# Optimization experiments

Hardware: AMD Instinct MI355X
Metric: run time of the kernel (lower is better)

The kernel has to match this reference:

```python
import jax, jax.numpy as jnp
import numpy as np

N_NODES = 50000
N_EDGES = 800000
N_GRAPHS = 64
IN_DIM = 108
HID = 128
OUT_DIM = 64


def setup_inputs() -> dict:
    key = jax.random.key(0)
    ks = jax.random.split(key, 10)
    x = jax.random.normal(ks[0], (N_NODES, IN_DIM - 1), dtype=jnp.float32)
    votes = jax.random.normal(ks[1], (N_NODES, 1), dtype=jnp.float32)
    edge_index = jax.random.randint(ks[2], (2, N_EDGES), 0, N_NODES, dtype=jnp.int64)
    batch = jnp.sort(jax.random.randint(ks[3], (N_NODES,), 0, N_GRAPHS, dtype=jnp.int64))
    # SAGEConv params (PyG defaults: mean aggr; lin_l has bias, lin_r has no bias)
    s1 = 1.0 / np.sqrt(IN_DIM)
    s2 = 1.0 / np.sqrt(HID)
    W1l = jax.random.uniform(ks[4], (IN_DIM, HID), jnp.float32, -s1, s1)
    b1 = jnp.zeros((HID,), jnp.float32)
    W1r = jax.random.uniform(ks[5], (IN_DIM, HID), jnp.float32, -s1, s1)
    W2l = jax.random.uniform(ks[6], (HID, OUT_DIM), jnp.float32, -s2, s2)
    b2 = jnp.zeros((OUT_DIM,), jnp.float32)
    W2r = jax.random.uniform(ks[7], (HID, OUT_DIM), jnp.float32, -s2, s2)
    return {"x": x, "votes": votes, "edge_index": edge_index, "batch": batch,
            "W1l": W1l, "b1": b1, "W1r": W1r, "W2l": W2l, "b2": b2, "W2r": W2r}


def _sage_conv(h, src, dst, Wl, b, Wr):
    # mean-aggregate neighbor features x_j at target i, then lin_l(agg) + lin_r(x_i)
    agg = jax.ops.segment_sum(h[src], dst, num_segments=h.shape[0])  # [N, d]
    deg = jax.ops.segment_sum(jnp.ones((src.shape[0],), h.dtype), dst,
                              num_segments=h.shape[0])
    agg = agg / jnp.maximum(deg, 1.0)[:, None]
    return agg @ Wl + b + h @ Wr


def reference(x, votes, edge_index, batch, W1l, b1, W1r, W2l, b2, W2r):
    src, dst = edge_index[0], edge_index[1]
    h = jnp.concatenate([x, votes], axis=1)              # [N, 108]
    h = jax.nn.relu(_sage_conv(h, src, dst, W1l, b1, W1r))  # [N, 128]
    h = _sage_conv(h, src, dst, W2l, b2, W2r)               # [N, 64]
    return jax.ops.segment_max(h, batch, num_segments=N_GRAPHS)  # [G, 64]
```

## Files before the change

### kernel.cpp

```cpp
#include <hip/hip_runtime.h>
#include <hip/hip_bf16.h>

#define IN_F 108
#define XD   107
#define HID  128
#define OUTD 64
#define SEG_NODES 64
#define BSH 6
#define BNODES 64
#define MAXBK 1024
#define EPB 4096
#define SRCMASK 0x03FFFFFF
#define BP1_N (8 * 7 * 64 * 8)
#define BP2_N (8 * 4 * 64 * 8)

typedef unsigned short ushort_t;
typedef unsigned int uint_t;
typedef __attribute__((ext_vector_type(8))) short bf16x8;
typedef __attribute__((ext_vector_type(4))) float f32x4;

__device__ inline void atomicMaxF(float* addr, float val) {
    if (val >= 0.f) atomicMax((int*)addr, __float_as_int(val));
    else            atomicMin((unsigned int*)addr, __float_as_uint(val));
}

__device__ inline ushort_t f2bf(float f) {
    uint_t b = __float_as_uint(f);
    return (ushort_t)((b + 0x7fffu + ((b >> 16) & 1u)) >> 16);
}

__global__ void init0_kernel(int* bcnt, int nbk, float* out, int n) {
    int i = blockIdx.x * 256 + threadIdx.x;
    if (i < nbk) bcnt[i] = 0;
    if (i < n) out[i] = -__builtin_inff();
}

__global__ __launch_bounds__(256) void bhist_kernel(const int* __restrict__ dst,
                                                    int* __restrict__ bcnt, int E, int nbk) {
    __shared__ int lh[MAXBK];
    for (int i = threadIdx.x; i < nbk; i += 256) lh[i] = 0;
    __syncthreads();
    int base = blockIdx.x * EPB;
    int end = min(base + EPB, E);
    for (int k = base + threadIdx.x; k < end; k += 256)
        atomicAdd(&lh[dst[k] >> BSH], 1);
    __syncthreads();
    for (int i = threadIdx.x; i < nbk; i += 256)
        if (lh[i] > 0) atomicAdd(&bcnt[i], lh[i]);
}

__global__ __launch_bounds__(64) void bscan_kernel(const int* __restrict__ bcnt,
                                                   int* __restrict__ bbase,
                                                   int* __restrict__ brsv,
                                                   int* __restrict__ row_start,
                                                   int nbk, int N, int E) {
    int lane = threadIdx.x;
    int carry = 0;
    for (int b = 0; b < nbk; b += 64) {
        int i = b + lane;
        int orig = (i < nbk) ? bcnt[i] : 0;
        int v = orig;
#pragma unroll
        for (int d = 1; d < 64; d <<= 1) {
            int t = __shfl_up(v, d);
            if (lane >= d) v += t;
        }
        if (i < nbk) {
            int ex = carry + v - orig;
            bbase[i] = ex;
            brsv[i] = ex;
        }
        carry += __shfl(v, 63);
    }
    if (lane == 0) {
        bbase[nbk] = E;
        row_start[N] = E;
    }
}

__global__ __launch_bounds__(256) void bscatter_kernel(const int* __restrict__ src,
                                                       const int* __restrict__ dst,
                                                       int* __restrict__ brsv,
                                                       uint_t* __restrict__ ebuf,
                                                       int E, int nbk) {
    __shared__ int lh[MAXBK];
    __shared__ int lofs[MAXBK];
    for (int i = threadIdx.x; i < nbk; i += 256) lh[i] = 0;
    __syncthreads();
    int base = blockIdx.x * EPB;
    int end = min(base + EPB, E);
    for (int k = base + threadIdx.x; k < end; k += 256)
        atomicAdd(&lh[dst[k] >> BSH], 1);
    __syncthreads();
    for (int i = threadIdx.x; i < nbk; i += 256)
        if (lh[i] > 0) lofs[i] = atomicAdd(&brsv[i], lh[i]);
    __syncthreads();
    for (int k = base + threadIdx.x; k < end; k += 256) {
        int d = dst[k];
        int pos = atomicAdd(&lofs[d >> BSH], 1);
        ebuf[pos] = (uint_t)src[k] | ((uint_t)(d & (BNODES - 1)) << 26);
    }
}

__global__ __launch_bounds__(256) void bbuild_kernel(const uint_t* __restrict__ ebuf,
                                                     const int* __restrict__ bbase,
                                                     int* __restrict__ row_start,
                                                     int* __restrict__ sorted_src,
                                                     int N) {
    __shared__ int nh[BNODES];
    __shared__ int cur[BNODES];
    int b = blockIdx.x;
    int e0 = bbase[b], e1 = bbase[b + 1];
    int nlo = b << BSH;
    int nloc = min(BNODES, N - nlo);
    if (threadIdx.x < BNODES) nh[threadIdx.x] = 0;
    __syncthreads();
    for (int k = e0 + threadIdx.x; k < e1; k += 256)
        atomicAdd(&nh[ebuf[k] >> 26], 1);
    __syncthreads();
    if (threadIdx.x < 64) {
        int lane = threadIdx.x;
        int orig = nh[lane];
        int v = orig;
#pragma unroll
        for (int d = 1; d < 64; d <<= 1) {
            int t = __shfl_up(v, d);
            if (lane >= d) v += t;
        }
        int ex = e0 + v - orig;
        cur[lane] = ex;
        if (lane < nloc) row_start[nlo + lane] = ex;
    }
    __syncthreads();
    for (int k = e0 + threadIdx.x; k < e1; k += 256) {
        uint_t e = ebuf[k];
        int pos = atomicAdd(&cur[e >> 26], 1);
        sorted_src[pos] = (int)(e & SRCMASK);
    }
}

__global__ void prep_kernel(const float* __restrict__ x, const float* __restrict__ votes,
                            const float* __restrict__ W1l, const float* __restrict__ W1r,
                            const float* __restrict__ W2l, const float* __restrict__ W2r,
                            ushort_t* __restrict__ xb, ushort_t* __restrict__ bp1,
                            ushort_t* __restrict__ bp2, int N) {
    int idx = blockIdx.x * 256 + threadIdx.x;
    if (idx < N * IN_F) {
        int n = idx / IN_F, f = idx - n * IN_F;
        float v = (f < XD) ? x[n * XD + f] : votes[n];
        xb[idx] = f2bf(v);
    }
    if (idx < BP1_N) {
        int j = idx & 7;
        int lane = (idx >> 3) & 63;
        int rest = idx >> 9;
        int ks = rest % 7;
        int ct = rest / 7;
        int k = ks * 32 + (lane >> 4) * 8 + j;
        int col = ct * 16 + (lane & 15);
        float v = 0.f;
        if (k < IN_F) v = W1l[k * HID + col];
        else if (k < 2 * IN_F) v = W1r[(k - IN_F) * HID + col];
        bp1[idx] = f2bf(v);
    }
    int i2 = idx - BP1_N;
    if (i2 >= 0 && i2 < BP2_N) {
        int j = i2 & 7;
        int lane = (i2 >> 3) & 63;
        int ks = (i2 >> 9) & 3;
        int ct = i2 >> 11;
        int k = ks * 32 + (lane >> 4) * 8 + j;
        int col = ct * 16 + (lane & 15);
        float v = (col < OUTD) ? W2l[k * OUTD + col] : W2r[k * OUTD + (col - OUTD)];
        bp2[i2] = f2bf(v);
    }
}

#define T1_M 32
#define A_STRIDE_US 232
#define A_STRIDE_U  116
#define H1_STRIDE_US 136
__global__ __launch_bounds__(256) void fused1_kernel(
        const ushort_t* __restrict__ xb,
        const int* __restrict__ row_start, const int* __restrict__ sorted_src,
        const ushort_t* __restrict__ bp1, const ushort_t* __restrict__ bp2,
        const float* __restrict__ b1,
        ushort_t* __restrict__ ub, float* __restrict__ vv, int N) {
    __shared__ uint_t smem[T1_M * A_STRIDE_U];
    int n0 = blockIdx.x * T1_M;
    const uint_t* xbu = (const uint_t*)xb;

    for (int i = threadIdx.x; i < T1_M * 54; i += 256) {
        int m = i / 54, c = i - m * 54;
        int n = n0 + m;
        smem[m * A_STRIDE_U + 54 + c] = (n < N) ? xbu[n * 54 + c] : 0u;
    }
    for (int i = threadIdx.x; i < T1_M * 4; i += 256) {
        int m = i >> 2, c = i & 3;
        smem[m * A_STRIDE_U + 108 + c] = 0u;
    }

    int lane = threadIdx.x & 63;
    int wid  = threadIdx.x >> 6;
    int h  = lane >> 5;
    int l2 = lane & 31;

    for (int it = 0; it < 8; ++it) {
        int m = wid * 8 + it;
        int node = n0 + m;
        float a0 = 0.f, a1 = 0.f, a2 = 0.f, a3 = 0.f;
        int deg = 0;
        if (node < N) {
            int rs = row_start[node], re = row_start[node + 1];
            deg = re - rs;
            for (int k0 = rs; k0 < re; k0 += 64) {
                int cnt = min(64, re - k0);
                int sl = sorted_src[k0 + min(lane, cnt - 1)];
                int t = 0;
                for (; t + 8 <= cnt; t += 8) {
                    int s0 = __shfl(sl, t + h);
                    int s1 = __shfl(sl, t + 2 + h);
                    int s2 = __shfl(sl, t + 4 + h);
                    int s3 = __shfl(sl, t + 6 + h);
                    if (l2 < 27) {
                        uint2 w0 = *(const uint2*)(xb + s0 * IN_F + 4 * l2);
                        uint2 w1 = *(const uint2*)(xb + s1 * IN_F + 4 * l2);
                        uint2 w2 = *(const uint2*)(xb + s2 * IN_F + 4 * l2);
                        uint2 w3 = *(const uint2*)(xb + s3 * IN_F + 4 * l2);
                        a0 += __uint_as_float(w0.x << 16) + __uint_as_float(w1.x << 16)
                            + __uint_as_float(w2.x << 16) + __uint_as_float(w3.x << 16);
                        a1 += __uint_as_float(w0.x & 0xffff0000u) + __uint_as_float(w1.x & 0xffff0000u)
                            + __uint_as_float(w2.x & 0xffff0000u) + __uint_as_float(w3.x & 0xffff0000u);
                        a2 += __uint_as_float(w0.y << 16) + __uint_as_float(w1.y << 16)
                            + __uint_as_float(w2.y << 16) + __uint_as_float(w3.y << 16);
                        a3 += __uint_as_float(w0.y & 0xffff0000u) + __uint_as_float(w1.y & 0xffff0000u)
                            + __uint_as_float(w2.y & 0xffff0000u) + __uint_as_float(w3.y & 0xffff0000u);
                    }
                }
                for (; t < cnt; t += 2) {
                    int tt = min(t + h, cnt - 1);
                    int s = __shfl(sl, tt);
                    if (t + h < cnt && l2 < 27) {
                        uint2 w = *(const uint2*)(xb + s * IN_F + 4 * l2);
                        a0 += __uint_as_float(w.x << 16);
                        a1 += __uint_as_float(w.x & 0xffff0000u);
                        a2 += __uint_as_float(w.y << 16);
                        a3 += __uint_as_float(w.y & 0xffff0000u);
                    }
                }
            }
        }
        a0 += __shfl_xor(a0, 32);
        a1 += __shfl_xor(a1, 32);
        a2 += __shfl_xor(a2, 32);
        a3 += __shfl_xor(a3, 32);
        if (node < N && l2 < 27) {
            float inv = 1.f / fmaxf((float)deg, 1.f);
            ushort4 p;
            p.x = f2bf(a0 * inv);
            p.y = f2bf(a1 * inv);
            p.z = f2bf(a2 * inv);
            p.w = f2bf(a3 * inv);
            *(ushort4*)((ushort_t*)smem + m * A_STRIDE_US + 4 * l2) = p;
        }
    }
    __syncthreads();

    int wrow = (wid & 1) << 4;
    int wcol = (wid >> 1) << 6;
    int arow = wrow + (lane & 15);
    int akoff = (lane >> 4) * 8;
    const ushort_t* sA = (const ushort_t*)smem;
    const bf16x8* bp1v = (const bf16x8*)bp1;

    f32x4 acc0 = {}, acc1 = {}, acc2_ = {}, acc3 = {};
    int ct0 = wcol >> 4;
#pragma unroll
    for (int ks = 0; ks < 7; ++ks) {
        bf16x8 af = *(const bf16x8*)(sA + arow * A_STRIDE_US + ks * 32 + akoff);
        bf16x8 bf0 = bp1v[((ct0 + 0) * 7 + ks) * 64 + lane];
        bf16x8 bf1 = bp1v[((ct0 + 1) * 7 + ks) * 64 + lane];
        bf16x8 bf2 = bp1v[((ct0 + 2) * 7 + ks) * 64 + lane];
        bf16x8 bf3 = bp1v[((ct0 + 3) * 7 + ks) * 64 + lane];
        acc0 = __builtin_amdgcn_mfma_f32_16x16x32_bf16(af, bf0, acc0, 0, 0, 0);
        acc1 = __builtin_amdgcn_mfma_f32_16x16x32_bf16(af, bf1, acc1, 0, 0, 0);
        acc2_ = __builtin_amdgcn_mfma_f32_16x16x32_bf16(af, bf2, acc2_, 0, 0, 0);
        acc3 = __builtin_amdgcn_mfma_f32_16x16x32_bf16(af, bf3, acc3, 0, 0, 0);
    }

    __syncthreads();
    ushort_t* sh1 = (ushort_t*)smem;
    {
        int colb = wcol + (lane & 15);
        int rowb = wrow + ((lane >> 4) << 2);
#pragma unroll
        for (int t = 0; t < 4; ++t) {
            f32x4 a = (t == 0) ? acc0 : (t == 1) ? acc1 : (t == 2) ? acc2_ : acc3;
            int col = colb + t * 16;
            float bj = b1[col];
#pragma unroll
            for (int r = 0; r < 4; ++r)
                sh1[(rowb + r) * H1_STRIDE_US + col] = f2bf(fmaxf(a[r] + bj, 0.f));
        }
    }
    __syncthreads();

    const bf16x8* bp2v = (const bf16x8*)bp2;
    f32x4 dcc0 = {}, dcc1 = {}, dcc2 = {}, dcc3 = {};
#pragma unroll
    for (int ks = 0; ks < 4; ++ks) {
        bf16x8 af = *(const bf16x8*)(sh1 + arow * H1_STRIDE_US + ks * 32 + akoff);
        bf16x8 bf0 = bp2v[((ct0 + 0) * 4 + ks) * 64 + lane];
        bf16x8 bf1 = bp2v[((ct0 + 1) * 4 + ks) * 64 + lane];
        bf16x8 bf2 = bp2v[((ct0 + 2) * 4 + ks) * 64 + lane];
        bf16x8 bf3 = bp2v[((ct0 + 3) * 4 + ks) * 64 + lane];
        dcc0 = __builtin_amdgcn_mfma_f32_16x16x32_bf16(af, bf0, dcc0, 0, 0, 0);
        dcc1 = __builtin_amdgcn_mfma_f32_16x16x32_bf16(af, bf1, dcc1, 0, 0, 0);
        dcc2 = __builtin_amdgcn_mfma_f32_16x16x32_bf16(af, bf2, dcc2, 0, 0, 0);
        dcc3 = __builtin_amdgcn_mfma_f32_16x16x32_bf16(af, bf3, dcc3, 0, 0, 0);
    }

    {
        int colb = wcol + (lane & 15);
        int rowb = wrow + ((lane >> 4) << 2);
#pragma unroll
        for (int t = 0; t < 4; ++t) {
            f32x4 a = (t == 0) ? dcc0 : (t == 1) ? dcc1 : (t == 2) ? dcc2 : dcc3;
            int col = colb + t * 16;
#pragma unroll
            for (int r = 0; r < 4; ++r) {
                int n = n0 + rowb + r;
                if (n < N) {
                    if (col < OUTD) ub[(n << 6) + col] = f2bf(a[r]);
                    else            vv[(n << 6) + (col - OUTD)] = a[r];
                }
            }
        }
    }
}

__global__ __launch_bounds__(256) void gatheru_kernel(
        const ushort_t* __restrict__ ub,
        const int* __restrict__ row_start, const int* __restrict__ sorted_src,
        float* __restrict__ aggu, int N) {
    int node = (blockIdx.x * 256 + threadIdx.x) >> 6;
    int lane = threadIdx.x & 63;
    if (node >= N) return;
    int rs = row_start[node], re = row_start[node + 1];
    int g  = lane >> 4;
    int l4 = lane & 15;
    float a0 = 0.f, a1 = 0.f, a2 = 0.f, a3 = 0.f;
    for (int k0 = rs; k0 < re; k0 += 64) {
        int cnt = min(64, re - k0);
        int sl = sorted_src[k0 + min(lane, cnt - 1)];
        int t = 0;
        for (; t + 8 <= cnt; t += 8) {
            int s0 = __shfl(sl, t + g);
            int s1 = __shfl(sl, t + 4 + g);
            uint2 w0 = *(const uint2*)(ub + (s0 << 6) + 4 * l4);
            uint2 w1 = *(const uint2*)(ub + (s1 << 6) + 4 * l4);
            a0 += __uint_as_float(w0.x << 16) + __uint_as_float(w1.x << 16);
            a1 += __uint_as_float(w0.x & 0xffff0000u) + __uint_as_float(w1.x & 0xffff0000u);
            a2 += __uint_as_float(w0.y << 16) + __uint_as_float(w1.y << 16);
            a3 += __uint_as_float(w0.y & 0xffff0000u) + __uint_as_float(w1.y & 0xffff0000u);
        }
        for (; t < cnt; t += 4) {
            int tt = min(t + g, cnt - 1);
            int s = __shfl(sl, tt);
            if (t + g < cnt) {
                uint2 w = *(const uint2*)(ub + (s << 6) + 4 * l4);
                a0 += __uint_as_float(w.x << 16);
                a1 += __uint_as_float(w.x & 0xffff0000u);
                a2 += __uint_as_float(w.y << 16);
                a3 += __uint_as_float(w.y & 0xffff0000u);
            }
        }
    }
    a0 += __shfl_xor(a0, 16); a0 += __shfl_xor(a0, 32);
    a1 += __shfl_xor(a1, 16); a1 += __shfl_xor(a1, 32);
    a2 += __shfl_xor(a2, 16); a2 += __shfl_xor(a2, 32);
    a3 += __shfl_xor(a3, 16); a3 += __shfl_xor(a3, 32);
    float inv = 1.f / fmaxf((float)(re - rs), 1.f);
    if (lane < 16) {
        *(float4*)(aggu + (node << 6) + 4 * lane) =
            make_float4(a0 * inv, a1 * inv, a2 * inv, a3 * inv);
    }
}

__global__ __launch_bounds__(256) void finalize_kernel(
        const float* __restrict__ aggu, const float* __restrict__ vv,
        const float* __restrict__ b2, const int* __restrict__ batch,
        float* __restrict__ out, int N) {
    int j  = threadIdx.x & 63;
    int nq = threadIdx.x >> 6;
    int n0 = blockIdx.x * SEG_NODES;
    float bj = b2[j];
    int curg = -1;
    float curm = -__builtin_inff();
    for (int m = nq; m < SEG_NODES; m += 4) {
        int n = n0 + m;
        if (n >= N) break;
        int g = batch[n];
        float v = aggu[(n << 6) + j] + vv[(n << 6) + j] + bj;
        if (g != curg) {
            if (curg >= 0) atomicMaxF(&out[(curg << 6) + j], curm);
            curg = g;
            curm = v;
        } else {
            curm = fmaxf(curm, v);
        }
    }
    if (curg >= 0) atomicMaxF(&out[(curg << 6) + j], curm);
}

static inline size_t align256(size_t v) { return (v + 255) & ~(size_t)255; }

extern "C" void kernel_launch(void* const* d_in, const int* in_sizes, int n_in,
                              void* d_out, int out_size, void* d_ws, size_t ws_size,
                              hipStream_t stream) {
    const float* x     = (const float*)d_in[0];
    const float* votes = (const float*)d_in[1];
    const int*   eidx  = (const int*)d_in[2];
    const int*   batch = (const int*)d_in[3];
    const float* W1l   = (const float*)d_in[4];
    const float* b1    = (const float*)d_in[5];
    const float* W1r   = (const float*)d_in[6];
    const float* W2l   = (const float*)d_in[7];
    const float* b2    = (const float*)d_in[8];
    const float* W2r   = (const float*)d_in[9];
    float* out = (float*)d_out;

    const int N = in_sizes[1];
    const int E = in_sizes[2] / 2;
    const int* src = eidx;
    const int* dst = eidx + E;
    const int nbk = (N + BNODES - 1) >> BSH;

    char* ws = (char*)d_ws;
    size_t off = 0;
    int* bcnt       = (int*)(ws + off); off = align256(off + (size_t)nbk * 4);
    int* bbase      = (int*)(ws + off); off = align256(off + (size_t)(nbk + 1) * 4);
    int* brsv       = (int*)(ws + off); off = align256(off + (size_t)nbk * 4);
    int* row_start  = (int*)(ws + off); off = align256(off + (size_t)(N + 1) * 4);
    uint_t* ebuf    = (uint_t*)(ws + off); off = align256(off + (size_t)E * 4);
    int* sorted_src = (int*)(ws + off); off = align256(off + (size_t)E * 4);
    ushort_t* xb    = (ushort_t*)(ws + off); off = align256(off + (size_t)N * IN_F * 2);
    ushort_t* ub    = (ushort_t*)(ws + off); off = align256(off + (size_t)N * OUTD * 2);
    float* vv       = (float*)(ws + off); off = align256(off + (size_t)N * OUTD * 4);
    float* aggu     = (float*)(ws + off); off = align256(off + (size_t)N * OUTD * 4);
    ushort_t* bp1   = (ushort_t*)(ws + off); off = align256(off + (size_t)BP1_N * 2);
    ushort_t* bp2   = (ushort_t*)(ws + off); off = align256(off + (size_t)BP2_N * 2);

    {
        int mx = max(nbk, out_size);
        init0_kernel<<<(mx + 255) / 256, 256, 0, stream>>>(bcnt, nbk, out, out_size);
    }

    int nebl = (E + EPB - 1) / EPB;
    bhist_kernel<<<nebl, 256, 0, stream>>>(dst, bcnt, E, nbk);
    bscan_kernel<<<1, 64, 0, stream>>>(bcnt, bbase, brsv, row_start, nbk, N, E);
    bscatter_kernel<<<nebl, 256, 0, stream>>>(src, dst, brsv, ebuf, E, nbk);
    bbuild_kernel<<<nbk, 256, 0, stream>>>(ebuf, bbase, row_start, sorted_src, N);

    prep_kernel<<<(N * IN_F + 255) / 256, 256, 0, stream>>>(x, votes, W1l, W1r, W2l, W2r,
                                                            xb, bp1, bp2, N);

    fused1_kernel<<<(N + T1_M - 1) / T1_M, 256, 0, stream>>>(xb, row_start, sorted_src,
                                                             bp1, bp2, b1, ub, vv, N);
    gatheru_kernel<<<(N + 3) / 4, 256, 0, stream>>>(ub, row_start, sorted_src, aggu, N);

    finalize_kernel<<<(N + SEG_NODES - 1) / SEG_NODES, 256, 0, stream>>>(
        aggu, vv, b2, batch, out, N);
}
```

Baseline: 132.8 us.

## Fuse setup kernels, prefetch neighbor lists, and merge gather with segment-max

Merges the dst histogram and the bf16 conversion/weight-packing prep into one launch, with a block-index split between the two jobs. In fused1, row_start values are cached in shared memory and the next node's neighbor indices are prefetched while the current node is processed. Bias b2 is folded into the stored vv term. The second-layer mean gather is fused with the graph-wise max reduction, so the aggu buffer and the finalize launch are removed. This cuts launches and one full N×64 fp32 round-trip, at the cost of fewer threads per node in the fused gather, with each wave now looping over 16 nodes.

Result: slower. 140.4 us (+5.7%).

```diff
diff --git a/kernel.cpp b/kernel.cpp
--- a/kernel.cpp
+++ b/kernel.cpp
@@ -5,7 +5,6 @@
 #define XD   107
 #define HID  128
 #define OUTD 64
-#define SEG_NODES 64
 #define BSH 6
 #define BNODES 64
 #define MAXBK 1024
@@ -35,18 +34,56 @@
     if (i < n) out[i] = -__builtin_inff();
 }
 
-__global__ __launch_bounds__(256) void bhist_kernel(const int* __restrict__ dst,
-                                                    int* __restrict__ bcnt, int E, int nbk) {
+__global__ __launch_bounds__(256) void setup_kernel(
+        const int* __restrict__ dst, int* __restrict__ bcnt, int E, int nbk, int nebl,
+        const float* __restrict__ x, const float* __restrict__ votes,
+        const float* __restrict__ W1l, const float* __restrict__ W1r,
+        const float* __restrict__ W2l, const float* __restrict__ W2r,
+        ushort_t* __restrict__ xb, ushort_t* __restrict__ bp1,
+        ushort_t* __restrict__ bp2, int N) {
     __shared__ int lh[MAXBK];
-    for (int i = threadIdx.x; i < nbk; i += 256) lh[i] = 0;
-    __syncthreads();
-    int base = blockIdx.x * EPB;
-    int end = min(base + EPB, E);
-    for (int k = base + threadIdx.x; k < end; k += 256)
-        atomicAdd(&lh[dst[k] >> BSH], 1);
-    __syncthreads();
-    for (int i = threadIdx.x; i < nbk; i += 256)
-        if (lh[i] > 0) atomicAdd(&bcnt[i], lh[i]);
+    if ((int)blockIdx.x < nebl) {
+        for (int i = threadIdx.x; i < nbk; i += 256) lh[i] = 0;
+        __syncthreads();
+        int base = blockIdx.x * EPB;
+        int end = min(base + EPB, E);
+        for (int k = base + threadIdx.x; k < end; k += 256)
+            atomicAdd(&lh[dst[k] >> BSH], 1);
+        __syncthreads();
+        for (int i = threadIdx.x; i < nbk; i += 256)
+            if (lh[i] > 0) atomicAdd(&bcnt[i], lh[i]);
+        return;
+    }
+    int idx = ((int)blockIdx.x - nebl) * 256 + threadIdx.x;
+    if (idx < N * IN_F) {
+        int n = idx / IN_F, f = idx - n * IN_F;
+        float v = (f < XD) ? x[n * XD + f] : votes[n];
+        xb[idx] = f2bf(v);
+    }
+    if (idx < BP1_N) {
+        int j = idx & 7;
+        int lane = (idx >> 3) & 63;
+        int rest = idx >> 9;
+        int ks = rest % 7;
+        int ct = rest / 7;
+        int k = ks * 32 + (lane >> 4) * 8 + j;
+        int col = ct * 16 + (lane & 15);
+        float v = 0.f;
+        if (k < IN_F) v = W1l[k * HID + col];
+        else if (k < 2 * IN_F) v = W1r[(k - IN_F) * HID + col];
+        bp1[idx] = f2bf(v);
+    }
+    int i2 = idx - BP1_N;
+    if (i2 >= 0 && i2 < BP2_N) {
+        int j = i2 & 7;
+        int lane = (i2 >> 3) & 63;
+        int ks = (i2 >> 9) & 3;
+        int ct = i2 >> 11;
+        int k = ks * 32 + (lane >> 4) * 8 + j;
+        int col = ct * 16 + (lane & 15);
+        float v = (col < OUTD) ? W2l[k * OUTD + col] : W2r[k * OUTD + (col - OUTD)];
+        bp2[i2] = f2bf(v);
+    }
 }
 
 __global__ __launch_bounds__(64) void bscan_kernel(const int* __restrict__ bcnt,
@@ -139,43 +176,6 @@
     }
 }
 
-__global__ void prep_kernel(const float* __restrict__ x, const float* __restrict__ votes,
-                            const float* __restrict__ W1l, const float* __restrict__ W1r,
-                            const float* __restrict__ W2l, const float* __restrict__ W2r,
-                            ushort_t* __restrict__ xb, ushort_t* __restrict__ bp1,
-                            ushort_t* __restrict__ bp2, int N) {
-    int idx = blockIdx.x * 256 + threadIdx.x;
-    if (idx < N * IN_F) {
-        int n = idx / IN_F, f = idx - n * IN_F;
-        float v = (f < XD) ? x[n * XD + f] : votes[n];
-        xb[idx] = f2bf(v);
-    }
-    if (idx < BP1_N) {
-        int j = idx & 7;
-        int lane = (idx >> 3) & 63;
-        int rest = idx >> 9;
-        int ks = rest % 7;
-        int ct = rest / 7;
-        int k = ks * 32 + (lane >> 4) * 8 + j;
-        int col = ct * 16 + (lane & 15);
-        float v = 0.f;
-        if (k < IN_F) v = W1l[k * HID + col];
-        else if (k < 2 * IN_F) v = W1r[(k - IN_F) * HID + col];
-        bp1[idx] = f2bf(v);
-    }
-    int i2 = idx - BP1_N;
-    if (i2 >= 0 && i2 < BP2_N) {
-        int j = i2 & 7;
-        int lane = (i2 >> 3) & 63;
-        int ks = (i2 >> 9) & 3;
-        int ct = i2 >> 11;
-        int k = ks * 32 + (lane >> 4) * 8 + j;
-        int col = ct * 16 + (lane & 15);
-        float v = (col < OUTD) ? W2l[k * OUTD + col] : W2r[k * OUTD + (col - OUTD)];
-        bp2[i2] = f2bf(v);
-    }
-}
-
 #define T1_M 32
 #define A_STRIDE_US 232
 #define A_STRIDE_U  116
@@ -184,9 +184,10 @@
         const ushort_t* __restrict__ xb,
         const int* __restrict__ row_start, const int* __restrict__ sorted_src,
         const ushort_t* __restrict__ bp1, const ushort_t* __restrict__ bp2,
-        const float* __restrict__ b1,
-        ushort_t* __restrict__ ub, float* __restrict__ vv, int N) {
+        const float* __restrict__ b1, const float* __restrict__ b2,
+        ushort_t* __restrict__ ub, float* __restrict__ vvb, int N) {
     __shared__ uint_t smem[T1_M * A_STRIDE_U];
+    __shared__ int rsh[T1_M + 1];
     int n0 = blockIdx.x * T1_M;
     const uint_t* xbu = (const uint_t*)xb;
 
@@ -199,54 +200,71 @@
         int m = i >> 2, c = i & 3;
         smem[m * A_STRIDE_U + 108 + c] = 0u;
     }
+    if (threadIdx.x <= T1_M) {
+        int n = n0 + threadIdx.x;
+        rsh[threadIdx.x] = row_start[min(n, N)];
+    }
+    __syncthreads();
 
     int lane = threadIdx.x & 63;
     int wid  = threadIdx.x >> 6;
     int h  = lane >> 5;
     int l2 = lane & 31;
 
+    int mq8 = wid * 8;
+    int sl_next = 0;
+    {
+        int rs0 = rsh[mq8], re0 = rsh[mq8 + 1];
+        if (re0 > rs0) {
+            int c = min(64, re0 - rs0);
+            sl_next = sorted_src[rs0 + min(lane, c - 1)];
+        }
+    }
     for (int it = 0; it < 8; ++it) {
-        int m = wid * 8 + it;
-        int node = n0 + m;
+        int m = mq8 + it;
+        int rs = rsh[m], re = rsh[m + 1];
+        int sl0 = sl_next;
+        if (it < 7) {
+            int rsn = rsh[m + 1], ren = rsh[m + 2];
+            if (ren > rsn) {
+                int c = min(64, ren - rsn);
+                sl_next = sorted_src[rsn + min(lane, c - 1)];
+            }
+        }
         float a0 = 0.f, a1 = 0.f, a2 = 0.f, a3 = 0.f;
-        int deg = 0;
-        if (node < N) {
-            int rs = row_start[node], re = row_start[node + 1];
-            deg = re - rs;
-            for (int k0 = rs; k0 < re; k0 += 64) {
-                int cnt = min(64, re - k0);
-                int sl = sorted_src[k0 + min(lane, cnt - 1)];
-                int t = 0;
-                for (; t + 8 <= cnt; t += 8) {
-                    int s0 = __shfl(sl, t + h);
-                    int s1 = __shfl(sl, t + 2 + h);
-                    int s2 = __shfl(sl, t + 4 + h);
-                    int s3 = __shfl(sl, t + 6 + h);
-                    if (l2 < 27) {
-                        uint2 w0 = *(const uint2*)(xb + s0 * IN_F + 4 * l2);
-                        uint2 w1 = *(const uint2*)(xb + s1 * IN_F + 4 * l2);
-                        uint2 w2 = *(const uint2*)(xb + s2 * IN_F + 4 * l2);
-                        uint2 w3 = *(const uint2*)(xb + s3 * IN_F + 4 * l2);
-                        a0 += __uint_as_float(w0.x << 16) + __uint_as_float(w1.x << 16)
-                            + __uint_as_float(w2.x << 16) + __uint_as_float(w3.x << 16);
-                        a1 += __uint_as_float(w0.x & 0xffff0000u) + __uint_as_float(w1.x & 0xffff0000u)
-                            + __uint_as_float(w2.x & 0xffff0000u) + __uint_as_float(w3.x & 0xffff0000u);
-                        a2 += __uint_as_float(w0.y << 16) + __uint_as_float(w1.y << 16)
-                            + __uint_as_float(w2.y << 16) + __uint_as_float(w3.y << 16);
-                        a3 += __uint_as_float(w0.y & 0xffff0000u) + __uint_as_float(w1.y & 0xffff0000u)
-                            + __uint_as_float(w2.y & 0xffff0000u) + __uint_as_float(w3.y & 0xffff0000u);
-                    }
+        for (int k0 = rs; k0 < re; k0 += 64) {
+            int cnt = min(64, re - k0);
+            int sl = (k0 == rs) ? sl0 : sorted_src[k0 + min(lane, cnt - 1)];
+            int t = 0;
+            for (; t + 8 <= cnt; t += 8) {
+                int s0 = __shfl(sl, t + h);
+                int s1 = __shfl(sl, t + 2 + h);
+                int s2 = __shfl(sl, t + 4 + h);
+                int s3 = __shfl(sl, t + 6 + h);
+                if (l2 < 27) {
+                    uint2 w0 = *(const uint2*)(xb + s0 * IN_F + 4 * l2);
+                    uint2 w1 = *(const uint2*)(xb + s1 * IN_F + 4 * l2);
+                    uint2 w2 = *(const uint2*)(xb + s2 * IN_F + 4 * l2);
+                    uint2 w3 = *(const uint2*)(xb + s3 * IN_F + 4 * l2);
+                    a0 += __uint_as_float(w0.x << 16) + __uint_as_float(w1.x << 16)
+                        + __uint_as_float(w2.x << 16) + __uint_as_float(w3.x << 16);
+                    a1 += __uint_as_float(w0.x & 0xffff0000u) + __uint_as_float(w1.x & 0xffff0000u)
+                        + __uint_as_float(w2.x & 0xffff0000u) + __uint_as_float(w3.x & 0xffff0000u);
+                    a2 += __uint_as_float(w0.y << 16) + __uint_as_float(w1.y << 16)
+                        + __uint_as_float(w2.y << 16) + __uint_as_float(w3.y << 16);
+                    a3 += __uint_as_float(w0.y & 0xffff0000u) + __uint_as_float(w1.y & 0xffff0000u)
+                        + __uint_as_float(w2.y & 0xffff0000u) + __uint_as_float(w3.y & 0xffff0000u);
                 }
-                for (; t < cnt; t += 2) {
-                    int tt = min(t + h, cnt - 1);
-                    int s = __shfl(sl, tt);
-                    if (t + h < cnt && l2 < 27) {
-                        uint2 w = *(const uint2*)(xb + s * IN_F + 4 * l2);
-                        a0 += __uint_as_float(w.x << 16);
-                        a1 += __uint_as_float(w.x & 0xffff0000u);
-                        a2 += __uint_as_float(w.y << 16);
-                        a3 += __uint_as_float(w.y & 0xffff0000u);
-                    }
+            }
+            for (; t < cnt; t += 2) {
+                int tt = min(t + h, cnt - 1);
+                int s = __shfl(sl, tt);
+                if (t + h < cnt && l2 < 27) {
+                    uint2 w = *(const uint2*)(xb + s * IN_F + 4 * l2);
+                    a0 += __uint_as_float(w.x << 16);
+                    a1 += __uint_as_float(w.x & 0xffff0000u);
+                    a2 += __uint_as_float(w.y << 16);
+                    a3 += __uint_as_float(w.y & 0xffff0000u);
                 }
             }
         }
@@ -254,8 +272,9 @@
         a1 += __shfl_xor(a1, 32);
         a2 += __shfl_xor(a2, 32);
         a3 += __shfl_xor(a3, 32);
+        int node = n0 + m;
         if (node < N && l2 < 27) {
-            float inv = 1.f / fmaxf((float)deg, 1.f);
+            float inv = 1.f / fmaxf((float)(re - rs), 1.f);
             ushort4 p;
             p.x = f2bf(a0 * inv);
             p.y = f2bf(a1 * inv);
@@ -331,86 +350,98 @@
             for (int r = 0; r < 4; ++r) {
                 int n = n0 + rowb + r;
                 if (n < N) {
-                    if (col < OUTD) ub[(n << 6) + col] = f2bf(a[r]);
-                    else            vv[(n << 6) + (col - OUTD)] = a[r];
+                    if (col < OUTD) {
+                        ub[(n << 6) + col] = f2bf(a[r]);
+                    } else {
+                        vvb[(n << 6) + (col - OUTD)] = a[r] + b2[col - OUTD];
+                    }
                 }
             }
         }
     }
 }
 
-__global__ __launch_bounds__(256) void gatheru_kernel(
+#define GF_NODES 64
+__global__ __launch_bounds__(256) void gatherf_kernel(
         const ushort_t* __restrict__ ub,
         const int* __restrict__ row_start, const int* __restrict__ sorted_src,
-        float* __restrict__ aggu, int N) {
-    int node = (blockIdx.x * 256 + threadIdx.x) >> 6;
+        const float* __restrict__ vvb, const int* __restrict__ batch,
+        float* __restrict__ out, int N) {
     int lane = threadIdx.x & 63;
-    if (node >= N) return;
-    int rs = row_start[node], re = row_start[node + 1];
-    int g  = lane >> 4;
+    int wid = threadIdx.x >> 6;
+    int nbase = blockIdx.x * GF_NODES + wid * 16;
+    int g4 = lane >> 4;
     int l4 = lane & 15;
-    float a0 = 0.f, a1 = 0.f, a2 = 0.f, a3 = 0.f;
-    for (int k0 = rs; k0 < re; k0 += 64) {
-        int cnt = min(64, re - k0);
-        int sl = sorted_src[k0 + min(lane, cnt - 1)];
-        int t = 0;
-        for (; t + 8 <= cnt; t += 8) {
-            int s0 = __shfl(sl, t + g);
-            int s1 = __shfl(sl, t + 4 + g);
-            uint2 w0 = *(const uint2*)(ub + (s0 << 6) + 4 * l4);
-            uint2 w1 = *(const uint2*)(ub + (s1 << 6) + 4 * l4);
-            a0 += __uint_as_float(w0.x << 16) + __uint_as_float(w1.x << 16);
-            a1 += __uint_as_float(w0.x & 0xffff0000u) + __uint_as_float(w1.x & 0xffff0000u);
-            a2 += __uint_as_float(w0.y << 16) + __uint_as_float(w1.y << 16);
-            a3 += __uint_as_float(w0.y & 0xffff0000u) + __uint_as_float(w1.y & 0xffff0000u);
-        }
-        for (; t < cnt; t += 4) {
-            int tt = min(t + g, cnt - 1);
-            int s = __shfl(sl, tt);
-            if (t + g < cnt) {
-                uint2 w = *(const uint2*)(ub + (s << 6) + 4 * l4);
-                a0 += __uint_as_float(w.x << 16);
-                a1 += __uint_as_float(w.x & 0xffff0000u);
-                a2 += __uint_as_float(w.y << 16);
-                a3 += __uint_as_float(w.y & 0xffff0000u);
-            }
-        }
-    }
-    a0 += __shfl_xor(a0, 16); a0 += __shfl_xor(a0, 32);
-    a1 += __shfl_xor(a1, 16); a1 += __shfl_xor(a1, 32);
-    a2 += __shfl_xor(a2, 16); a2 += __shfl_xor(a2, 32);
-    a3 += __shfl_xor(a3, 16); a3 += __shfl_xor(a3, 32);
-    float inv = 1.f / fmaxf((float)(re - rs), 1.f);
-    if (lane < 16) {
-        *(float4*)(aggu + (node << 6) + 4 * lane) =
-            make_float4(a0 * inv, a1 * inv, a2 * inv, a3 * inv);
-    }
-}
-
-__global__ __launch_bounds__(256) void finalize_kernel(
-        const float* __restrict__ aggu, const float* __restrict__ vv,
-        const float* __restrict__ b2, const int* __restrict__ batch,
-        float* __restrict__ out, int N) {
-    int j  = threadIdx.x & 63;
-    int nq = threadIdx.x >> 6;
-    int n0 = blockIdx.x * SEG_NODES;
-    float bj = b2[j];
     int curg = -1;
-    float curm = -__builtin_inff();
-    for (int m = nq; m < SEG_NODES; m += 4) {
-        int n = n0 + m;
-        if (n >= N) break;
-        int g = batch[n];
-        float v = aggu[(n << 6) + j] + vv[(n << 6) + j] + bj;
-        if (g != curg) {
-            if (curg >= 0) atomicMaxF(&out[(curg << 6) + j], curm);
-            curg = g;
-            curm = v;
-        } else {
-            curm = fmaxf(curm, v);
-        }
-    }
-    if (curg >= 0) atomicMaxF(&out[(curg << 6) + j], curm);
+    float m0 = 0.f, m1 = 0.f, m2 = 0.f, m3 = 0.f;
+    for (int it = 0; it < 16; ++it) {
+        int node = nbase + it;
+        if (node >= N) break;
+        int rs = row_start[node], re = row_start[node + 1];
+        float a0 = 0.f, a1 = 0.f, a2 = 0.f, a3 = 0.f;
+        for (int k0 = rs; k0 < re; k0 += 64) {
+            int cnt = min(64, re - k0);
+            int sl = sorted_src[k0 + min(lane, cnt - 1)];
+            int t = 0;
+            for (; t + 8 <= cnt; t += 8) {
+                int s0 = __shfl(sl, t + g4);
+                int s1 = __shfl(sl, t + 4 + g4);
+                uint2 w0 = *(const uint2*)(ub + (s0 << 6) + 4 * l4);
+                uint2 w1 = *(const uint2*)(ub + (s1 << 6) + 4 * l4);
+                a0 += __uint_as_float(w0.x << 16) + __uint_as_float(w1.x << 16);
+                a1 += __uint_as_float(w0.x & 0xffff0000u) + __uint_as_float(w1.x & 0xffff0000u);
+                a2 += __uint_as_float(w0.y << 16) + __uint_as_float(w1.y << 16);
+                a3 += __uint_as_float(w0.y & 0xffff0000u) + __uint_as_float(w1.y & 0xffff0000u);
+            }
+            for (; t < cnt; t += 4) {
+                int tt = min(t + g4, cnt - 1);
+                int s = __shfl(sl, tt);
+                if (t + g4 < cnt) {
+                    uint2 w = *(const uint2*)(ub + (s << 6) + 4 * l4);
+                    a0 += __uint_as_float(w.x << 16);
+                    a1 += __uint_as_float(w.x & 0xffff0000u);
+                    a2 += __uint_as_float(w.y << 16);
+                    a3 += __uint_as_float(w.y & 0xffff0000u);
+                }
+            }
+        }
+        a0 += __shfl_xor(a0, 16); a0 += __shfl_xor(a0, 32);
+        a1 += __shfl_xor(a1, 16); a1 += __shfl_xor(a1, 32);
+        a2 += __shfl_xor(a2, 16); a2 += __shfl_xor(a2, 32);
+        a3 += __shfl_xor(a3, 16); a3 += __shfl_xor(a3, 32);
+        if (lane < 16) {
+            float inv = 1.f / fmaxf((float)(re - rs), 1.f);
+            float4 vb = *(const float4*)(vvb + (node << 6) + 4 * l4);
+            float h0v = a0 * inv + vb.x;
+            float h1v = a1 * inv + vb.y;
+            float h2v = a2 * inv + vb.z;
+            float h3v = a3 * inv + vb.w;
+            int g = batch[node];
+            if (g != curg) {
+                if (curg >= 0) {
+                    float* o = out + (curg << 6) + 4 * l4;
+                    atomicMaxF(o + 0, m0);
+                    atomicMaxF(o + 1, m1);
+                    atomicMaxF(o + 2, m2);
+                    atomicMaxF(o + 3, m3);
+                }
+                curg = g;
+                m0 = h0v; m1 = h1v; m2 = h2v; m3 = h3v;
+            } else {
+                m0 = fmaxf(m0, h0v);
+                m1 = fmaxf(m1, h1v);
+                m2 = fmaxf(m2, h2v);
+                m3 = fmaxf(m3, h3v);
+            }
+        }
+    }
+    if (lane < 16 && curg >= 0) {
+        float* o = out + (curg << 6) + 4 * l4;
+        atomicMaxF(o + 0, m0);
+        atomicMaxF(o + 1, m1);
+        atomicMaxF(o + 2, m2);
+        atomicMaxF(o + 3, m3);
+    }
 }
 
 static inline size_t align256(size_t v) { return (v + 255) & ~(size_t)255; }
@@ -446,8 +477,7 @@
     int* sorted_src = (int*)(ws + off); off = align256(off + (size_t)E * 4);
     ushort_t* xb    = (ushort_t*)(ws + off); off = align256(off + (size_t)N * IN_F * 2);
     ushort_t* ub    = (ushort_t*)(ws + off); off = align256(off + (size_t)N * OUTD * 2);
-    float* vv       = (float*)(ws + off); off = align256(off + (size_t)N * OUTD * 4);
-    float* aggu     = (float*)(ws + off); off = align256(off + (size_t)N * OUTD * 4);
+    float* vvb      = (float*)(ws + off); off = align256(off + (size_t)N * OUTD * 4);
     ushort_t* bp1   = (ushort_t*)(ws + off); off = align256(off + (size_t)BP1_N * 2);
     ushort_t* bp2   = (ushort_t*)(ws + off); off = align256(off + (size_t)BP2_N * 2);
 
@@ -457,18 +487,17 @@
     }
 
     int nebl = (E + EPB - 1) / EPB;
-    bhist_kernel<<<nebl, 256, 0, stream>>>(dst, bcnt, E, nbk);
+    int prep_blocks = (N * IN_F + 255) / 256;
+    setup_kernel<<<nebl + prep_blocks, 256, 0, stream>>>(dst, bcnt, E, nbk, nebl,
+                                                         x, votes, W1l, W1r, W2l, W2r,
+                                                         xb, bp1, bp2, N);
+
     bscan_kernel<<<1, 64, 0, stream>>>(bcnt, bbase, brsv, row_start, nbk, N, E);
     bscatter_kernel<<<nebl, 256, 0, stream>>>(src, dst, brsv, ebuf, E, nbk);
     bbuild_kernel<<<nbk, 256, 0, stream>>>(ebuf, bbase, row_start, sorted_src, N);
 
-    prep_kernel<<<(N * IN_F + 255) / 256, 256, 0, stream>>>(x, votes, W1l, W1r, W2l, W2r,
-                                                            xb, bp1, bp2, N);
-
     fused1_kernel<<<(N + T1_M - 1) / T1_M, 256, 0, stream>>>(xb, row_start, sorted_src,
-                                                             bp1, bp2, b1, ub, vv, N);
-    gatheru_kernel<<<(N + 3) / 4, 256, 0, stream>>>(ub, row_start, sorted_src, aggu, N);
-
-    finalize_kernel<<<(N + SEG_NODES - 1) / SEG_NODES, 256, 0, stream>>>(
-        aggu, vv, b2, batch, out, N);
-}
+                                                             bp1, bp2, b1, b2, ub, vvb, N);
+    gatherf_kernel<<<(N + GF_NODES - 1) / GF_NODES, 256, 0, stream>>>(
+        ub, row_start, sorted_src, vvb, batch, out, N);
+}
```
